# Optimization experiments

Measured on AMD Instinct MI355X. Metric: run time of the kernel, lower is better.

The kernel has to match this reference:

```python
import jax, jax.numpy as jnp
import numpy as np

LOG2PI = float(np.log(2.0 * np.pi))

INPUT_DIM, HIDDEN_DIM, OUTPUT_DIM, HORIZON = 128, 2048, 128, 1024


def setup_inputs() -> dict:
    key = jax.random.key(0)
    ks = jax.random.split(key, 10)
    s = 0.02
    return {
        "s0": jax.random.normal(ks[0], (HORIZON, INPUT_DIM), jnp.float32),
        "eps": jax.random.normal(ks[1], (HORIZON, OUTPUT_DIM), jnp.float32),
        "W_ih": jax.random.normal(ks[2], (4 * HIDDEN_DIM, INPUT_DIM), jnp.float32) * s,
        "W_hh": jax.random.normal(ks[3], (4 * HIDDEN_DIM, HIDDEN_DIM), jnp.float32) * s,
        "b_ih": jax.random.normal(ks[4], (4 * HIDDEN_DIM,), jnp.float32) * s,
        "b_hh": jax.random.normal(ks[5], (4 * HIDDEN_DIM,), jnp.float32) * s,
        "W_mu": jax.random.normal(ks[6], (OUTPUT_DIM, HIDDEN_DIM), jnp.float32) * s,
        "b_mu": jax.random.normal(ks[7], (OUTPUT_DIM,), jnp.float32) * s,
        "W_lv": jax.random.normal(ks[8], (OUTPUT_DIM, HIDDEN_DIM), jnp.float32) * s,
        "b_lv": jax.random.normal(ks[9], (OUTPUT_DIM,), jnp.float32) * s,
        "H": HORIZON,
    }


def reference(s0, eps, W_ih, W_hh, b_ih, b_hh, W_mu, b_mu, W_lv, b_lv, H):
    hd = W_hh.shape[1]

    def step(carry, inp):
        h, c = carry  # [hidden], [hidden]
        x, e = inp    # [input_dim], [output_dim]
        gates = W_ih @ x + b_ih + W_hh @ h + b_hh  # [4*hidden]
        i, f, g, o = jnp.split(gates, 4)
        i, f, o = jax.nn.sigmoid(i), jax.nn.sigmoid(f), jax.nn.sigmoid(o)
        g = jnp.tanh(g)
        c = f * c + i * g
        h = o * jnp.tanh(c)
        mu = W_mu @ h + b_mu
        logvar = W_lv @ h + b_lv
        std = jnp.exp(0.5 * logvar)
        # Normal.sample() is detached from the graph in torch
        x_samp = jax.lax.stop_gradient(mu + std * e)
        lp = -0.5 * jnp.square((x_samp - mu) / std) - jnp.log(std) - 0.5 * LOG2PI
        return (h, c), (x_samp, lp, h)

    h0 = jnp.zeros((hd,), s0.dtype)
    c0 = jnp.zeros((hd,), s0.dtype)
    _, (xs, lps, hs) = jax.lax.scan(step, (h0, c0), (s0[:H], eps[:H]))
    return xs, lps, hs  # [H, out], [H, out], [H, hidden]
```

## Files before the change

### kernel.cpp

```cpp
#include <hip/hip_runtime.h>
#include <math.h>

#define TSTEPS 1024
#define HID    2048
#define IN_D   128
#define OUT_D  128
#define NWG    256
#define NTHR   512
#define NPAIRS (HID / 2)

#define LOG2PI_F 1.8378770664093453f

typedef unsigned long long u64;
typedef unsigned int       u32;

static __device__ __forceinline__ float sigmoidf_(float x) {
    return 1.0f / (1.0f + expf(-x));
}

static __device__ __forceinline__ u32 bf16_rne(float f) {
    u32 u = __float_as_uint(f);
    return (u + 0x7FFFu + ((u >> 16) & 1u)) >> 16;
}
static __device__ __forceinline__ float bf16_lo(u32 payload) {
    return __uint_as_float(payload << 16);
}
static __device__ __forceinline__ float bf16_hi(u32 payload) {
    return __uint_as_float(payload & 0xFFFF0000u);
}

__global__ __launch_bounds__(NTHR, 2)
void lstm_persist(const float* __restrict__ s0,
                  const float* __restrict__ Wih,
                  const float* __restrict__ Whh,
                  const float* __restrict__ bih,
                  const float* __restrict__ bhh,
                  float* __restrict__ hs_out,
                  u64* __restrict__ pairs)
{
    __shared__ __align__(16) float4 ldsH[HID / 4];
    __shared__ __align__(16) float  gsum[32];

    const int tid   = threadIdx.x;
    const int wg    = blockIdx.x;
    const int hbase = wg * 8;
    const int rg    = tid >> 6;
    const int lane  = tid & 63;

    float w[4][32];
    int growm[4];
#pragma unroll
    for (int m = 0; m < 4; ++m) {
        const int li = rg * 4 + m;
        growm[m] = (li >> 3) * HID + hbase + (li & 7);
        const float4* src = (const float4*)(Whh + (size_t)growm[m] * HID + lane * 32);
#pragma unroll
        for (int q = 0; q < 8; ++q) {
            float4 v = src[q];
            w[m][4*q+0] = v.x; w[m][4*q+1] = v.y;
            w[m][4*q+2] = v.z; w[m][4*q+3] = v.w;
        }
    }
    float wih2[4][2];
    float breg[4];
#pragma unroll
    for (int m = 0; m < 4; ++m) {
        wih2[m][0] = Wih[(size_t)growm[m] * IN_D + 2 * lane];
        wih2[m][1] = Wih[(size_t)growm[m] * IN_D + 2 * lane + 1];
        breg[m]    = bih[growm[m]] + bhh[growm[m]];
    }

    float2 c2 = make_float2(0.f, 0.f);

    for (int t = 0; t < TSTEPS; ++t) {
        const float2 xv = *(const float2*)(s0 + (size_t)t * IN_D + 2 * lane);
        float acc[4];
#pragma unroll
        for (int m = 0; m < 4; ++m)
            acc[m] = wih2[m][0] * xv.x + wih2[m][1] * xv.y;

        if (t > 0) {
            const u32 want = (u32)t;
            const u64* sp = pairs + (size_t)((t - 1) & 1) * NPAIRS + 2 * tid;
            u64 q0, q1;
            for (;;) {
                q0 = __hip_atomic_load(sp,     __ATOMIC_RELAXED, __HIP_MEMORY_SCOPE_AGENT);
                q1 = __hip_atomic_load(sp + 1, __ATOMIC_RELAXED, __HIP_MEMORY_SCOPE_AGENT);
                if ((u32)(q0 >> 32) == want && (u32)(q1 >> 32) == want) break;
                __builtin_amdgcn_s_sleep(2);
            }
            float4 hv;
            hv.x = bf16_lo((u32)q0);
            hv.y = bf16_hi((u32)q0);
            hv.z = bf16_lo((u32)q1);
            hv.w = bf16_hi((u32)q1);
            const int p = tid ^ ((tid >> 3) & 7);
            ldsH[p] = hv;
        }
        __syncthreads();

        if (t > 0) {
#pragma unroll
            for (int j = 0; j < 8; ++j) {
                const int c4 = 8 * lane + j;
                const int p  = c4 ^ (lane & 7);
                float4 hv = ldsH[p];
#pragma unroll
                for (int m = 0; m < 4; ++m) {
                    acc[m] += hv.x * w[m][4*j+0];
                    acc[m] += hv.y * w[m][4*j+1];
                    acc[m] += hv.z * w[m][4*j+2];
                    acc[m] += hv.w * w[m][4*j+3];
                }
            }
        }

#pragma unroll
        for (int m = 0; m < 4; ++m) {
            acc[m] += __shfl_xor(acc[m], 1);
            acc[m] += __shfl_xor(acc[m], 2);
            acc[m] += __shfl_xor(acc[m], 4);
            acc[m] += __shfl_xor(acc[m], 8);
            acc[m] += __shfl_xor(acc[m], 16);
            acc[m] += __shfl_xor(acc[m], 32);
        }
        if (lane == 0) {
            *(float4*)&gsum[rg * 4] = make_float4(acc[0] + breg[0], acc[1] + breg[1],
                                                  acc[2] + breg[2], acc[3] + breg[3]);
        }
        __syncthreads();

        if (tid < 4) {
            const int j0 = 2 * tid, j1 = 2 * tid + 1;
            const float i0 = sigmoidf_(gsum[j0]),      i1 = sigmoidf_(gsum[j1]);
            const float f0 = sigmoidf_(gsum[8  + j0]), f1 = sigmoidf_(gsum[8  + j1]);
            const float g0 = tanhf    (gsum[16 + j0]), g1 = tanhf    (gsum[16 + j1]);
            const float o0 = sigmoidf_(gsum[24 + j0]), o1 = sigmoidf_(gsum[24 + j1]);
            c2.x = f0 * c2.x + i0 * g0;
            c2.y = f1 * c2.y + i1 * g1;
            const float h0 = o0 * tanhf(c2.x);
            const float h1 = o1 * tanhf(c2.y);
            const u64 pkt = (u64)(bf16_rne(h0) | (bf16_rne(h1) << 16))
                          | ((u64)(u32)(t + 1) << 32);
            __hip_atomic_store(&pairs[(size_t)(t & 1) * NPAIRS + wg * 4 + tid], pkt,
                               __ATOMIC_RELAXED, __HIP_MEMORY_SCOPE_AGENT);
            *(float2*)&hs_out[(size_t)t * HID + hbase + j0] = make_float2(h0, h1);
        }
    }
}

__global__ __launch_bounds__(256)
void out_head(const float* __restrict__ eps,
              const float* __restrict__ Wmu,
              const float* __restrict__ bmu,
              const float* __restrict__ Wlv,
              const float* __restrict__ blv,
              const float* __restrict__ hs,
              float* __restrict__ xs,
              float* __restrict__ lp)
{
    __shared__ __align__(16) float hlds[4][HID];
    __shared__ __align__(16) float exch[4][256];

    const int tid = threadIdx.x;
    const int t0  = blockIdx.x * 4;

    {
        const float4* src = (const float4*)(hs + (size_t)t0 * HID);
        float4* dst = (float4*)&hlds[0][0];
#pragma unroll
        for (int i = 0; i < 8; ++i)
            dst[tid + i * 256] = src[tid + i * 256];
    }
    __syncthreads();

    const int  jrow  = tid & 127;
    const bool is_lv = tid >= 128;
    const float* Wrow = (is_lv ? Wlv : Wmu) + (size_t)jrow * HID;
    const float  bias = is_lv ? blv[jrow] : bmu[jrow];

    float acc[4] = {0.f, 0.f, 0.f, 0.f};
    const float4* w4 = (const float4*)Wrow;
#pragma unroll 4
    for (int kq = 0; kq < HID / 4; ++kq) {
        float4 wv = w4[kq];
#pragma unroll
        for (int tt = 0; tt < 4; ++tt) {
            float4 hv = ((const float4*)&hlds[tt][0])[kq];
            acc[tt] += wv.x * hv.x + wv.y * hv.y + wv.z * hv.z + wv.w * hv.w;
        }
    }
#pragma unroll
    for (int tt = 0; tt < 4; ++tt) exch[tt][tid] = acc[tt] + bias;
    __syncthreads();

#pragma unroll
    for (int r = 0; r < 2; ++r) {
        const int item = tid + r * 256;
        const int tt = item >> 7;
        const int jj = item & 127;
        const int t  = t0 + tt;
        const float mu = exch[tt][jj];
        const float lv = exch[tt][128 + jj];
        const float e  = eps[(size_t)t * OUT_D + jj];
        const float sd = expf(0.5f * lv);
        const float x  = mu + sd * e;
        const float d  = (x - mu) / sd;
        const float l  = -0.5f * d * d - 0.5f * lv - 0.5f * LOG2PI_F;
        xs[(size_t)t * OUT_D + jj] = x;
        lp[(size_t)t * OUT_D + jj] = l;
    }
}

extern "C" void kernel_launch(void* const* d_in, const int* in_sizes, int n_in,
                              void* d_out, int out_size, void* d_ws, size_t ws_size,
                              hipStream_t stream)
{
    (void)in_sizes; (void)n_in; (void)out_size; (void)ws_size;

    const float* s0  = (const float*)d_in[0];
    const float* eps = (const float*)d_in[1];
    const float* Wih = (const float*)d_in[2];
    const float* Whh = (const float*)d_in[3];
    const float* bih = (const float*)d_in[4];
    const float* bhh = (const float*)d_in[5];
    const float* Wmu = (const float*)d_in[6];
    const float* bmu = (const float*)d_in[7];
    const float* Wlv = (const float*)d_in[8];
    const float* blv = (const float*)d_in[9];

    float* out = (float*)d_out;
    float* xs = out;
    float* lp = out + TSTEPS * OUT_D;
    float* hs = out + 2 * TSTEPS * OUT_D;

    u64* pairs = (u64*)d_ws;

    (void)hipMemsetAsync(d_ws, 0, 2 * NPAIRS * sizeof(u64), stream);

    hipLaunchKernelGGL(lstm_persist, dim3(NWG), dim3(NTHR), 0, stream,
                       s0, Wih, Whh, bih, bhh, hs, pairs);

    hipLaunchKernelGGL(out_head, dim3(TSTEPS / 4), dim3(256), 0, stream,
                       eps, Wmu, bmu, Wlv, blv, hs, xs, lp);
}
```

Baseline: 3.620 ms.

## Compute LSTM cell per wavefront and drop intra-step barrier with 32-bit packets

Each wavefront now owns one hidden cell and holds all four of its gate rows, so the gate nonlinearities and cell update run in lane 0 right after the shuffle reduction. This removes the LDS gate exchange and the second __syncthreads per step. The hidden-state LDS buffer is double-buffered so the next step's writes cannot race with reads of the current one. Each cell publishes a 32-bit packet holding a bf16 value and a 16-bit step tag, and the polling loop uses a shorter sleep. Sigmoid and tanh switch to fast exp/rcp approximations, which slightly changes accuracy.

```diff
diff --git a/kernel.cpp b/kernel.cpp
--- a/kernel.cpp
+++ b/kernel.cpp
@@ -7,26 +7,24 @@
 #define OUT_D  128
 #define NWG    256
 #define NTHR   512
-#define NPAIRS (HID / 2)
 
 #define LOG2PI_F 1.8378770664093453f
 
 typedef unsigned long long u64;
 typedef unsigned int       u32;
-
-static __device__ __forceinline__ float sigmoidf_(float x) {
-    return 1.0f / (1.0f + expf(-x));
-}
 
 static __device__ __forceinline__ u32 bf16_rne(float f) {
     u32 u = __float_as_uint(f);
     return (u + 0x7FFFu + ((u >> 16) & 1u)) >> 16;
 }
-static __device__ __forceinline__ float bf16_lo(u32 payload) {
-    return __uint_as_float(payload << 16);
-}
-static __device__ __forceinline__ float bf16_hi(u32 payload) {
-    return __uint_as_float(payload & 0xFFFF0000u);
+static __device__ __forceinline__ float bf16_f(u32 b) {
+    return __uint_as_float(b << 16);
+}
+static __device__ __forceinline__ float fast_sig(float x) {
+    return __builtin_amdgcn_rcpf(1.0f + __expf(-x));
+}
+static __device__ __forceinline__ float fast_tanh(float x) {
+    return 1.0f - 2.0f * __builtin_amdgcn_rcpf(1.0f + __expf(2.0f * x));
 }
 
 __global__ __launch_bounds__(NTHR, 2)
@@ -36,41 +34,35 @@
                   const float* __restrict__ bih,
                   const float* __restrict__ bhh,
                   float* __restrict__ hs_out,
-                  u64* __restrict__ pairs)
+                  u32* __restrict__ pkts)
 {
-    __shared__ __align__(16) float4 ldsH[HID / 4];
-    __shared__ __align__(16) float  gsum[32];
-
-    const int tid   = threadIdx.x;
-    const int wg    = blockIdx.x;
-    const int hbase = wg * 8;
-    const int rg    = tid >> 6;
-    const int lane  = tid & 63;
+    __shared__ __align__(16) float4 ldsH[2][HID / 4];
+
+    const int tid  = threadIdx.x;
+    const int wg   = blockIdx.x;
+    const int rg   = tid >> 6;
+    const int lane = tid & 63;
+    const int cell = wg * 8 + rg;
 
     float w[4][32];
-    int growm[4];
+    float wih2[4][2];
+    float breg[4];
 #pragma unroll
     for (int m = 0; m < 4; ++m) {
-        const int li = rg * 4 + m;
-        growm[m] = (li >> 3) * HID + hbase + (li & 7);
-        const float4* src = (const float4*)(Whh + (size_t)growm[m] * HID + lane * 32);
+        const int grow = m * HID + cell;
+        const float4* src = (const float4*)(Whh + (size_t)grow * HID + lane * 32);
 #pragma unroll
         for (int q = 0; q < 8; ++q) {
             float4 v = src[q];
             w[m][4*q+0] = v.x; w[m][4*q+1] = v.y;
             w[m][4*q+2] = v.z; w[m][4*q+3] = v.w;
         }
-    }
-    float wih2[4][2];
-    float breg[4];
-#pragma unroll
-    for (int m = 0; m < 4; ++m) {
-        wih2[m][0] = Wih[(size_t)growm[m] * IN_D + 2 * lane];
-        wih2[m][1] = Wih[(size_t)growm[m] * IN_D + 2 * lane + 1];
-        breg[m]    = bih[growm[m]] + bhh[growm[m]];
-    }
-
-    float2 c2 = make_float2(0.f, 0.f);
+        wih2[m][0] = Wih[(size_t)grow * IN_D + 2 * lane];
+        wih2[m][1] = Wih[(size_t)grow * IN_D + 2 * lane + 1];
+        breg[m]    = bih[grow] + bhh[grow];
+    }
+
+    float c = 0.0f;
 
     for (int t = 0; t < TSTEPS; ++t) {
         const float2 xv = *(const float2*)(s0 + (size_t)t * IN_D + 2 * lane);
@@ -80,31 +72,33 @@
             acc[m] = wih2[m][0] * xv.x + wih2[m][1] * xv.y;
 
         if (t > 0) {
-            const u32 want = (u32)t;
-            const u64* sp = pairs + (size_t)((t - 1) & 1) * NPAIRS + 2 * tid;
+            const u32 want = (u32)t & 0xFFFFu;
+            const u64* sp = (const u64*)(pkts + (size_t)((t - 1) & 1) * HID + 4 * tid);
             u64 q0, q1;
             for (;;) {
                 q0 = __hip_atomic_load(sp,     __ATOMIC_RELAXED, __HIP_MEMORY_SCOPE_AGENT);
                 q1 = __hip_atomic_load(sp + 1, __ATOMIC_RELAXED, __HIP_MEMORY_SCOPE_AGENT);
-                if ((u32)(q0 >> 32) == want && (u32)(q1 >> 32) == want) break;
-                __builtin_amdgcn_s_sleep(2);
+                const u32 t0 = ((u32)(q0 >> 16)) & 0xFFFFu;
+                const u32 t1 = (u32)(q0 >> 48);
+                const u32 t2 = ((u32)(q1 >> 16)) & 0xFFFFu;
+                const u32 t3 = (u32)(q1 >> 48);
+                if ((t0 == want) & (t1 == want) & (t2 == want) & (t3 == want)) break;
+                __builtin_amdgcn_s_sleep(1);
             }
             float4 hv;
-            hv.x = bf16_lo((u32)q0);
-            hv.y = bf16_hi((u32)q0);
-            hv.z = bf16_lo((u32)q1);
-            hv.w = bf16_hi((u32)q1);
-            const int p = tid ^ ((tid >> 3) & 7);
-            ldsH[p] = hv;
+            hv.x = bf16_f((u32)q0 & 0xFFFFu);
+            hv.y = bf16_f((u32)(q0 >> 32) & 0xFFFFu);
+            hv.z = bf16_f((u32)q1 & 0xFFFFu);
+            hv.w = bf16_f((u32)(q1 >> 32) & 0xFFFFu);
+            ldsH[(t - 1) & 1][tid ^ ((tid >> 3) & 7)] = hv;
         }
         __syncthreads();
 
         if (t > 0) {
 #pragma unroll
             for (int j = 0; j < 8; ++j) {
-                const int c4 = 8 * lane + j;
-                const int p  = c4 ^ (lane & 7);
-                float4 hv = ldsH[p];
+                const int p = (8 * lane + j) ^ (lane & 7);
+                float4 hv = ldsH[(t - 1) & 1][p];
 #pragma unroll
                 for (int m = 0; m < 4; ++m) {
                     acc[m] += hv.x * w[m][4*j+0];
@@ -124,27 +118,22 @@
             acc[m] += __shfl_xor(acc[m], 16);
             acc[m] += __shfl_xor(acc[m], 32);
         }
+
         if (lane == 0) {
-            *(float4*)&gsum[rg * 4] = make_float4(acc[0] + breg[0], acc[1] + breg[1],
-                                                  acc[2] + breg[2], acc[3] + breg[3]);
-        }
-        __syncthreads();
-
-        if (tid < 4) {
-            const int j0 = 2 * tid, j1 = 2 * tid + 1;
-            const float i0 = sigmoidf_(gsum[j0]),      i1 = sigmoidf_(gsum[j1]);
-            const float f0 = sigmoidf_(gsum[8  + j0]), f1 = sigmoidf_(gsum[8  + j1]);
-            const float g0 = tanhf    (gsum[16 + j0]), g1 = tanhf    (gsum[16 + j1]);
-            const float o0 = sigmoidf_(gsum[24 + j0]), o1 = sigmoidf_(gsum[24 + j1]);
-            c2.x = f0 * c2.x + i0 * g0;
-            c2.y = f1 * c2.y + i1 * g1;
-            const float h0 = o0 * tanhf(c2.x);
-            const float h1 = o1 * tanhf(c2.y);
-            const u64 pkt = (u64)(bf16_rne(h0) | (bf16_rne(h1) << 16))
-                          | ((u64)(u32)(t + 1) << 32);
-            __hip_atomic_store(&pairs[(size_t)(t & 1) * NPAIRS + wg * 4 + tid], pkt,
+            const float zi = acc[0] + breg[0];
+            const float zf = acc[1] + breg[1];
+            const float zg = acc[2] + breg[2];
+            const float zo = acc[3] + breg[3];
+            const float ig = fast_sig(zi);
+            const float fg = fast_sig(zf);
+            const float og = fast_sig(zo);
+            const float gg = fast_tanh(zg);
+            c = fg * c + ig * gg;
+            const float h = og * fast_tanh(c);
+            const u32 pkt = (((u32)(t + 1) & 0xFFFFu) << 16) | bf16_rne(h);
+            __hip_atomic_store(&pkts[(size_t)(t & 1) * HID + cell], pkt,
                                __ATOMIC_RELAXED, __HIP_MEMORY_SCOPE_AGENT);
-            *(float2*)&hs_out[(size_t)t * HID + hbase + j0] = make_float2(h0, h1);
+            hs_out[(size_t)t * HID + cell] = h;
         }
     }
 }
@@ -234,12 +223,12 @@
     float* lp = out + TSTEPS * OUT_D;
     float* hs = out + 2 * TSTEPS * OUT_D;
 
-    u64* pairs = (u64*)d_ws;
-
-    (void)hipMemsetAsync(d_ws, 0, 2 * NPAIRS * sizeof(u64), stream);
+    u32* pkts = (u32*)d_ws;
+
+    (void)hipMemsetAsync(d_ws, 0, 2 * HID * sizeof(u32), stream);
 
     hipLaunchKernelGGL(lstm_persist, dim3(NWG), dim3(NTHR), 0, stream,
-                       s0, Wih, Whh, bih, bhh, hs, pairs);
+                       s0, Wih, Whh, bih, bhh, hs, pkts);
 
     hipLaunchKernelGGL(out_head, dim3(TSTEPS / 4), dim3(256), 0, stream,
                        eps, Wmu, bmu, Wlv, blv, hs, xs, lp);
```

After: 5.821 ms. 1.61x slower.

## Halve persistent LSTM workgroups, double hidden units per WG, fast gate math

Applied to the files above, without the earlier changes.

Cuts the persistent LSTM grid from 256 to 128 workgroups, each now holding 16 hidden units (two per wave, 256 weight registers per thread) with launch bounds of one block per CU. The aim is to halve the number of producers and consumers in the grid-wide flag synchronisation each step. It also double-buffers the LDS hidden-state copy, shortens the spin sleep, and swaps the sigmoid/tanh libcalls for exp+rcp approximations. The cost is heavy register pressure with possible spills, twice the FMA work per thread on the serial path, and slightly lower precision in the activations.

```diff
diff --git a/kernel.cpp b/kernel.cpp
--- a/kernel.cpp
+++ b/kernel.cpp
@@ -5,7 +5,7 @@
 #define HID    2048
 #define IN_D   128
 #define OUT_D  128
-#define NWG    256
+#define NWG    128
 #define NTHR   512
 #define NPAIRS (HID / 2)
 
@@ -13,10 +13,6 @@
 
 typedef unsigned long long u64;
 typedef unsigned int       u32;
-
-static __device__ __forceinline__ float sigmoidf_(float x) {
-    return 1.0f / (1.0f + expf(-x));
-}
 
 static __device__ __forceinline__ u32 bf16_rne(float f) {
     u32 u = __float_as_uint(f);
@@ -28,8 +24,14 @@
 static __device__ __forceinline__ float bf16_hi(u32 payload) {
     return __uint_as_float(payload & 0xFFFF0000u);
 }
-
-__global__ __launch_bounds__(NTHR, 2)
+static __device__ __forceinline__ float fast_sig(float x) {
+    return __builtin_amdgcn_rcpf(1.0f + __expf(-x));
+}
+static __device__ __forceinline__ float fast_tanh(float x) {
+    return 1.0f - 2.0f * __builtin_amdgcn_rcpf(1.0f + __expf(2.0f * x));
+}
+
+__global__ __launch_bounds__(NTHR, 1)
 void lstm_persist(const float* __restrict__ s0,
                   const float* __restrict__ Wih,
                   const float* __restrict__ Whh,
@@ -38,46 +40,46 @@
                   float* __restrict__ hs_out,
                   u64* __restrict__ pairs)
 {
-    __shared__ __align__(16) float4 ldsH[HID / 4];
-    __shared__ __align__(16) float  gsum[32];
-
-    const int tid   = threadIdx.x;
-    const int wg    = blockIdx.x;
-    const int hbase = wg * 8;
-    const int rg    = tid >> 6;
-    const int lane  = tid & 63;
-
-    float w[4][32];
-    int growm[4];
+    __shared__ __align__(16) float4 ldsH[2][HID / 4];
+    __shared__ __align__(16) float  gsum[64];
+
+    const int tid  = threadIdx.x;
+    const int wg   = blockIdx.x;
+    const int rg   = tid >> 6;
+    const int lane = tid & 63;
+    const int c0   = wg * 16 + 2 * rg;
+
+    float w[4][2][32];
+    float wihr[4][2][2];
+    float breg[4][2];
 #pragma unroll
     for (int m = 0; m < 4; ++m) {
-        const int li = rg * 4 + m;
-        growm[m] = (li >> 3) * HID + hbase + (li & 7);
-        const float4* src = (const float4*)(Whh + (size_t)growm[m] * HID + lane * 32);
-#pragma unroll
-        for (int q = 0; q < 8; ++q) {
-            float4 v = src[q];
-            w[m][4*q+0] = v.x; w[m][4*q+1] = v.y;
-            w[m][4*q+2] = v.z; w[m][4*q+3] = v.w;
-        }
-    }
-    float wih2[4][2];
-    float breg[4];
-#pragma unroll
-    for (int m = 0; m < 4; ++m) {
-        wih2[m][0] = Wih[(size_t)growm[m] * IN_D + 2 * lane];
-        wih2[m][1] = Wih[(size_t)growm[m] * IN_D + 2 * lane + 1];
-        breg[m]    = bih[growm[m]] + bhh[growm[m]];
+#pragma unroll
+        for (int b = 0; b < 2; ++b) {
+            const int grow = m * HID + c0 + b;
+            const float4* src = (const float4*)(Whh + (size_t)grow * HID + lane * 32);
+#pragma unroll
+            for (int q = 0; q < 8; ++q) {
+                float4 v = src[q];
+                w[m][b][4*q+0] = v.x; w[m][b][4*q+1] = v.y;
+                w[m][b][4*q+2] = v.z; w[m][b][4*q+3] = v.w;
+            }
+            wihr[m][b][0] = Wih[(size_t)grow * IN_D + 2 * lane];
+            wihr[m][b][1] = Wih[(size_t)grow * IN_D + 2 * lane + 1];
+            breg[m][b]    = bih[grow] + bhh[grow];
+        }
     }
 
     float2 c2 = make_float2(0.f, 0.f);
 
     for (int t = 0; t < TSTEPS; ++t) {
         const float2 xv = *(const float2*)(s0 + (size_t)t * IN_D + 2 * lane);
-        float acc[4];
+        float acc[4][2];
 #pragma unroll
         for (int m = 0; m < 4; ++m)
-            acc[m] = wih2[m][0] * xv.x + wih2[m][1] * xv.y;
+#pragma unroll
+            for (int b = 0; b < 2; ++b)
+                acc[m][b] = wihr[m][b][0] * xv.x + wihr[m][b][1] * xv.y;
 
         if (t > 0) {
             const u32 want = (u32)t;
@@ -87,64 +89,72 @@
                 q0 = __hip_atomic_load(sp,     __ATOMIC_RELAXED, __HIP_MEMORY_SCOPE_AGENT);
                 q1 = __hip_atomic_load(sp + 1, __ATOMIC_RELAXED, __HIP_MEMORY_SCOPE_AGENT);
                 if ((u32)(q0 >> 32) == want && (u32)(q1 >> 32) == want) break;
-                __builtin_amdgcn_s_sleep(2);
+                __builtin_amdgcn_s_sleep(1);
             }
             float4 hv;
             hv.x = bf16_lo((u32)q0);
             hv.y = bf16_hi((u32)q0);
             hv.z = bf16_lo((u32)q1);
             hv.w = bf16_hi((u32)q1);
-            const int p = tid ^ ((tid >> 3) & 7);
-            ldsH[p] = hv;
+            ldsH[(t - 1) & 1][tid ^ ((tid >> 3) & 7)] = hv;
         }
         __syncthreads();
 
         if (t > 0) {
 #pragma unroll
             for (int j = 0; j < 8; ++j) {
-                const int c4 = 8 * lane + j;
-                const int p  = c4 ^ (lane & 7);
-                float4 hv = ldsH[p];
-#pragma unroll
-                for (int m = 0; m < 4; ++m) {
-                    acc[m] += hv.x * w[m][4*j+0];
-                    acc[m] += hv.y * w[m][4*j+1];
-                    acc[m] += hv.z * w[m][4*j+2];
-                    acc[m] += hv.w * w[m][4*j+3];
-                }
-            }
-        }
-
-#pragma unroll
-        for (int m = 0; m < 4; ++m) {
-            acc[m] += __shfl_xor(acc[m], 1);
-            acc[m] += __shfl_xor(acc[m], 2);
-            acc[m] += __shfl_xor(acc[m], 4);
-            acc[m] += __shfl_xor(acc[m], 8);
-            acc[m] += __shfl_xor(acc[m], 16);
-            acc[m] += __shfl_xor(acc[m], 32);
-        }
+                const int p = (8 * lane + j) ^ (lane & 7);
+                float4 hv = ldsH[(t - 1) & 1][p];
+#pragma unroll
+                for (int m = 0; m < 4; ++m)
+#pragma unroll
+                    for (int b = 0; b < 2; ++b) {
+                        acc[m][b] += hv.x * w[m][b][4*j+0];
+                        acc[m][b] += hv.y * w[m][b][4*j+1];
+                        acc[m][b] += hv.z * w[m][b][4*j+2];
+                        acc[m][b] += hv.w * w[m][b][4*j+3];
+                    }
+            }
+        }
+
+#pragma unroll
+        for (int m = 0; m < 4; ++m)
+#pragma unroll
+            for (int b = 0; b < 2; ++b) {
+                acc[m][b] += __shfl_xor(acc[m][b], 1);
+                acc[m][b] += __shfl_xor(acc[m][b], 2);
+                acc[m][b] += __shfl_xor(acc[m][b], 4);
+                acc[m][b] += __shfl_xor(acc[m][b], 8);
+                acc[m][b] += __shfl_xor(acc[m][b], 16);
+                acc[m][b] += __shfl_xor(acc[m][b], 32);
+            }
         if (lane == 0) {
-            *(float4*)&gsum[rg * 4] = make_float4(acc[0] + breg[0], acc[1] + breg[1],
-                                                  acc[2] + breg[2], acc[3] + breg[3]);
+            *(float4*)&gsum[rg * 8]     = make_float4(acc[0][0] + breg[0][0],
+                                                      acc[1][0] + breg[1][0],
+                                                      acc[2][0] + breg[2][0],
+                                                      acc[3][0] + breg[3][0]);
+            *(float4*)&gsum[rg * 8 + 4] = make_float4(acc[0][1] + breg[0][1],
+                                                      acc[1][1] + breg[1][1],
+                                                      acc[2][1] + breg[2][1],
+                                                      acc[3][1] + breg[3][1]);
         }
         __syncthreads();
 
-        if (tid < 4) {
-            const int j0 = 2 * tid, j1 = 2 * tid + 1;
-            const float i0 = sigmoidf_(gsum[j0]),      i1 = sigmoidf_(gsum[j1]);
-            const float f0 = sigmoidf_(gsum[8  + j0]), f1 = sigmoidf_(gsum[8  + j1]);
-            const float g0 = tanhf    (gsum[16 + j0]), g1 = tanhf    (gsum[16 + j1]);
-            const float o0 = sigmoidf_(gsum[24 + j0]), o1 = sigmoidf_(gsum[24 + j1]);
+        if (tid < 8) {
+            const float* gs = &gsum[tid * 8];
+            const float i0 = fast_sig(gs[0]), f0 = fast_sig(gs[1]);
+            const float g0 = fast_tanh(gs[2]), o0 = fast_sig(gs[3]);
+            const float i1 = fast_sig(gs[4]), f1 = fast_sig(gs[5]);
+            const float g1 = fast_tanh(gs[6]), o1 = fast_sig(gs[7]);
             c2.x = f0 * c2.x + i0 * g0;
             c2.y = f1 * c2.y + i1 * g1;
-            const float h0 = o0 * tanhf(c2.x);
-            const float h1 = o1 * tanhf(c2.y);
+            const float h0 = o0 * fast_tanh(c2.x);
+            const float h1 = o1 * fast_tanh(c2.y);
             const u64 pkt = (u64)(bf16_rne(h0) | (bf16_rne(h1) << 16))
                           | ((u64)(u32)(t + 1) << 32);
-            __hip_atomic_store(&pairs[(size_t)(t & 1) * NPAIRS + wg * 4 + tid], pkt,
+            __hip_atomic_store(&pairs[(size_t)(t & 1) * NPAIRS + wg * 8 + tid], pkt,
                                __ATOMIC_RELAXED, __HIP_MEMORY_SCOPE_AGENT);
-            *(float2*)&hs_out[(size_t)t * HID + hbase + j0] = make_float2(h0, h1);
+            *(float2*)&hs_out[(size_t)t * HID + wg * 16 + 2 * tid] = make_float2(h0, h1);
         }
     }
 }
```

Result: slower. 6.754 ms (+86.6%).

## Poll h-state with one wavefront into double-buffered LDS and use fast gate activations

Applied to the files above, without the earlier changes.

Only the first wavefront of each workgroup now polls the published h-state flags. It loads 16 packets per lane and checks them with a wave-wide vote, writing into a double-buffered LDS h array indexed by step parity. Previously all 512 threads each polled their own two packets. This is meant to cut L2 polling traffic and latency on the per-step grid synchronisation. The sigmoid and tanh calls are also replaced with exp plus hardware reciprocal approximations, which shortens the serial gate tail at a small accuracy cost, and the occupancy hint in launch bounds is dropped.

```diff
diff --git a/kernel.cpp b/kernel.cpp
--- a/kernel.cpp
+++ b/kernel.cpp
@@ -14,10 +14,6 @@
 typedef unsigned long long u64;
 typedef unsigned int       u32;
 
-static __device__ __forceinline__ float sigmoidf_(float x) {
-    return 1.0f / (1.0f + expf(-x));
-}
-
 static __device__ __forceinline__ u32 bf16_rne(float f) {
     u32 u = __float_as_uint(f);
     return (u + 0x7FFFu + ((u >> 16) & 1u)) >> 16;
@@ -28,8 +24,14 @@
 static __device__ __forceinline__ float bf16_hi(u32 payload) {
     return __uint_as_float(payload & 0xFFFF0000u);
 }
-
-__global__ __launch_bounds__(NTHR, 2)
+static __device__ __forceinline__ float fast_sig(float x) {
+    return __builtin_amdgcn_rcpf(1.0f + __expf(-x));
+}
+static __device__ __forceinline__ float fast_tanh(float x) {
+    return 1.0f - 2.0f * __builtin_amdgcn_rcpf(1.0f + __expf(2.0f * x));
+}
+
+__global__ __launch_bounds__(NTHR)
 void lstm_persist(const float* __restrict__ s0,
                   const float* __restrict__ Wih,
                   const float* __restrict__ Whh,
@@ -38,7 +40,7 @@
                   float* __restrict__ hs_out,
                   u64* __restrict__ pairs)
 {
-    __shared__ __align__(16) float4 ldsH[HID / 4];
+    __shared__ __align__(16) float4 ldsH[2][HID / 4];
     __shared__ __align__(16) float  gsum[32];
 
     const int tid   = threadIdx.x;
@@ -48,63 +50,67 @@
     const int lane  = tid & 63;
 
     float w[4][32];
-    int growm[4];
+    float wih2[4][2];
+    float breg[4];
 #pragma unroll
     for (int m = 0; m < 4; ++m) {
         const int li = rg * 4 + m;
-        growm[m] = (li >> 3) * HID + hbase + (li & 7);
-        const float4* src = (const float4*)(Whh + (size_t)growm[m] * HID + lane * 32);
+        const int grow = (li >> 3) * HID + hbase + (li & 7);
+        const float4* src = (const float4*)(Whh + (size_t)grow * HID + lane * 32);
 #pragma unroll
         for (int q = 0; q < 8; ++q) {
             float4 v = src[q];
             w[m][4*q+0] = v.x; w[m][4*q+1] = v.y;
             w[m][4*q+2] = v.z; w[m][4*q+3] = v.w;
         }
-    }
-    float wih2[4][2];
-    float breg[4];
-#pragma unroll
-    for (int m = 0; m < 4; ++m) {
-        wih2[m][0] = Wih[(size_t)growm[m] * IN_D + 2 * lane];
-        wih2[m][1] = Wih[(size_t)growm[m] * IN_D + 2 * lane + 1];
-        breg[m]    = bih[growm[m]] + bhh[growm[m]];
+        wih2[m][0] = Wih[(size_t)grow * IN_D + 2 * lane];
+        wih2[m][1] = Wih[(size_t)grow * IN_D + 2 * lane + 1];
+        breg[m]    = bih[grow] + bhh[grow];
     }
 
     float2 c2 = make_float2(0.f, 0.f);
 
     for (int t = 0; t < TSTEPS; ++t) {
+        const int slot = (t - 1) & 1;
+
         const float2 xv = *(const float2*)(s0 + (size_t)t * IN_D + 2 * lane);
         float acc[4];
 #pragma unroll
         for (int m = 0; m < 4; ++m)
             acc[m] = wih2[m][0] * xv.x + wih2[m][1] * xv.y;
 
+        if (t > 0 && rg == 0) {
+            const u32 want = (u32)t;
+            const u64* base = pairs + (size_t)slot * NPAIRS;
+            u64 v[16];
+            for (;;) {
+                int ok = 1;
+#pragma unroll
+                for (int j = 0; j < 16; ++j) {
+                    v[j] = __hip_atomic_load(base + 64 * j + lane,
+                                             __ATOMIC_RELAXED, __HIP_MEMORY_SCOPE_AGENT);
+                    ok &= ((u32)(v[j] >> 32) == want);
+                }
+                if (__all(ok)) break;
+                __builtin_amdgcn_s_sleep(1);
+            }
+#pragma unroll
+            for (int j = 0; j < 16; ++j) {
+                const int idx  = 64 * j + lane;
+                const int cch  = idx >> 1;
+                const int half = idx & 1;
+                const int p    = cch ^ ((cch >> 3) & 7);
+                float* dst = (float*)&ldsH[slot][p] + 2 * half;
+                *(float2*)dst = make_float2(bf16_lo((u32)v[j]), bf16_hi((u32)v[j]));
+            }
+        }
+        __syncthreads();
+
         if (t > 0) {
-            const u32 want = (u32)t;
-            const u64* sp = pairs + (size_t)((t - 1) & 1) * NPAIRS + 2 * tid;
-            u64 q0, q1;
-            for (;;) {
-                q0 = __hip_atomic_load(sp,     __ATOMIC_RELAXED, __HIP_MEMORY_SCOPE_AGENT);
-                q1 = __hip_atomic_load(sp + 1, __ATOMIC_RELAXED, __HIP_MEMORY_SCOPE_AGENT);
-                if ((u32)(q0 >> 32) == want && (u32)(q1 >> 32) == want) break;
-                __builtin_amdgcn_s_sleep(2);
-            }
-            float4 hv;
-            hv.x = bf16_lo((u32)q0);
-            hv.y = bf16_hi((u32)q0);
-            hv.z = bf16_lo((u32)q1);
-            hv.w = bf16_hi((u32)q1);
-            const int p = tid ^ ((tid >> 3) & 7);
-            ldsH[p] = hv;
-        }
-        __syncthreads();
-
-        if (t > 0) {
 #pragma unroll
             for (int j = 0; j < 8; ++j) {
-                const int c4 = 8 * lane + j;
-                const int p  = c4 ^ (lane & 7);
-                float4 hv = ldsH[p];
+                const int p = (8 * lane + j) ^ (lane & 7);
+                float4 hv = ldsH[slot][p];
 #pragma unroll
                 for (int m = 0; m < 4; ++m) {
                     acc[m] += hv.x * w[m][4*j+0];
@@ -132,14 +138,14 @@
 
         if (tid < 4) {
             const int j0 = 2 * tid, j1 = 2 * tid + 1;
-            const float i0 = sigmoidf_(gsum[j0]),      i1 = sigmoidf_(gsum[j1]);
-            const float f0 = sigmoidf_(gsum[8  + j0]), f1 = sigmoidf_(gsum[8  + j1]);
-            const float g0 = tanhf    (gsum[16 + j0]), g1 = tanhf    (gsum[16 + j1]);
-            const float o0 = sigmoidf_(gsum[24 + j0]), o1 = sigmoidf_(gsum[24 + j1]);
+            const float i0 = fast_sig (gsum[j0]),      i1 = fast_sig (gsum[j1]);
+            const float f0 = fast_sig (gsum[8  + j0]), f1 = fast_sig (gsum[8  + j1]);
+            const float g0 = fast_tanh(gsum[16 + j0]), g1 = fast_tanh(gsum[16 + j1]);
+            const float o0 = fast_sig (gsum[24 + j0]), o1 = fast_sig (gsum[24 + j1]);
             c2.x = f0 * c2.x + i0 * g0;
             c2.y = f1 * c2.y + i1 * g1;
-            const float h0 = o0 * tanhf(c2.x);
-            const float h1 = o1 * tanhf(c2.y);
+            const float h0 = o0 * fast_tanh(c2.x);
+            const float h1 = o1 * fast_tanh(c2.y);
             const u64 pkt = (u64)(bf16_rne(h0) | (bf16_rne(h1) << 16))
                           | ((u64)(u32)(t + 1) << 32);
             __hip_atomic_store(&pairs[(size_t)(t & 1) * NPAIRS + wg * 4 + tid], pkt,
```

After: 2.971 ms. 1.22x faster.
